# Kernel optimization log

Measured on AMD Instinct MI355X. Metric: run time of the kernel, lower is better.

## Reference

```python
import jax, jax.numpy as jnp
import numpy as np

DIM = 512
HEADS = 8
HD = DIM // HEADS          # head_dim = 64
GROUPS = 32                # GroupNorm groups
EPS = 1e-5
SCALE = HD ** -0.25        # double-scale: applied to both q and k
B, H, W, L, CTX = 8, 32, 32, 77, 768


def setup_inputs() -> dict:
    key = jax.random.key(0)
    ks = jax.random.split(key, 6)
    return {
        "x": jax.random.normal(ks[0], (B, DIM, H, W), jnp.float32),
        "context": jax.random.normal(ks[1], (B, L, CTX), jnp.float32),
        "gn_gamma": jnp.ones((DIM,), jnp.float32),
        "gn_beta": jnp.zeros((DIM,), jnp.float32),
        "qkv_w": jax.random.normal(ks[2], (3 * DIM, DIM), jnp.float32) * 0.02,
        "qkv_b": jnp.zeros((3 * DIM,), jnp.float32),
        "ckv_w": jax.random.normal(ks[3], (2 * DIM, CTX), jnp.float32) * 0.02,
        "ckv_b": jnp.zeros((2 * DIM,), jnp.float32),
        "proj_w": jax.random.normal(ks[4], (DIM, DIM), jnp.float32) * 0.02,
        "proj_b": jnp.zeros((DIM,), jnp.float32),
    }


def _group_norm(x, gamma, beta):
    b, c, h, w = x.shape
    xr = x.reshape(b, GROUPS, c // GROUPS, h, w)
    mu = xr.mean(axis=(2, 3, 4), keepdims=True)
    var = xr.var(axis=(2, 3, 4), keepdims=True)
    xr = (xr - mu) * jax.lax.rsqrt(var + EPS)
    return xr.reshape(b, c, h, w) * gamma[None, :, None, None] + beta[None, :, None, None]


def reference(x, context, gn_gamma, gn_beta, qkv_w, qkv_b, ckv_w, ckv_b, proj_w, proj_b):
    b, c, h, w = x.shape
    n, d = HEADS, HD
    identity = x

    xn = _group_norm(x, gn_gamma, gn_beta)
    # 1x1 conv == channel GEMM. qkv: [b, 3*dim, h*w] -> [b, 3, n, d, hw]
    qkv = jnp.einsum('bchw,oc->bohw', xn, qkv_w) + qkv_b[None, :, None, None]
    qkv = qkv.reshape(b, 3, n, d, h * w)
    q, k, v = qkv[:, 0], qkv[:, 1], qkv[:, 2]   # each [b, n, d, hw]

    # context kv: Linear(context_dim, 2*dim) -> [b, L, 2, n, d] -> [b, n, d, L]
    ckv = jnp.einsum('blc,oc->blo', context, ckv_w) + ckv_b
    ckv = ckv.reshape(b, -1, 2, n, d)
    ck = jnp.transpose(ckv[:, :, 0], (0, 2, 3, 1))  # [b, n, d, L]
    cv = jnp.transpose(ckv[:, :, 1], (0, 2, 3, 1))
    k = jnp.concatenate([ck, k], axis=-1)           # [b, n, d, L+hw]
    v = jnp.concatenate([cv, v], axis=-1)

    # attn = (q^T * s) @ (k * s); softmax over keys
    attn = jnp.einsum('bndq,bndk->bnqk', q * SCALE, k * SCALE)
    attn = jax.nn.softmax(attn, axis=-1)
    out = jnp.einsum('bndk,bnqk->bndq', v, attn).reshape(b, c, h, w)

    out = jnp.einsum('bchw,oc->bohw', out, proj_w) + proj_b[None, :, None, None]
    return out + identity
```

## Files before the change

### kernel.cpp

```cpp
#include <hip/hip_runtime.h>

#define B_ 8
#define DIM_ 512
#define HEADS_ 8
#define HD_ 64
#define HW_ 1024
#define L_ 77
#define LP_ 80
#define CTX_ 768
#define KV_ 1101
#define KVP_ 1152
#define NPAD_ 51
#define CTX0_ 1024
#define SC_QK 0.42466089f

typedef __attribute__((ext_vector_type(8))) short bf16x8;
typedef __attribute__((ext_vector_type(4))) float f32x4;
typedef __attribute__((ext_vector_type(4))) unsigned short u16x4;

__device__ __forceinline__ unsigned short f2bf(float f) {
  union { float f; unsigned int u; } c; c.f = f;
  unsigned int u = c.u;
  return (unsigned short)((u + 0x7fffu + ((u >> 16) & 1u)) >> 16);
}
__device__ __forceinline__ float bf2f(unsigned short h) {
  union { unsigned int u; float f; } c; c.u = ((unsigned int)h) << 16;
  return c.f;
}

#define GLD_LDS16(gsrc, ldst) \
  __builtin_amdgcn_global_load_lds((const __attribute__((address_space(1))) void*)(gsrc), \
                                   (__attribute__((address_space(3))) void*)(ldst), 16, 0, 0)

__global__ __launch_bounds__(256) void prep_k(const float* __restrict__ qkv_w,
                                              const float* __restrict__ ckv_w,
                                              const float* __restrict__ proj_w,
                                              const float* __restrict__ ctx,
                                              unsigned short* __restrict__ dq,
                                              unsigned short* __restrict__ dc,
                                              unsigned short* __restrict__ dp,
                                              unsigned short* __restrict__ ctx_bf,
                                              unsigned short* __restrict__ k_s,
                                              unsigned short* __restrict__ vT) {
  int bid = blockIdx.x;
  int tid = threadIdx.x;
  if (bid < 1792) {
    int i = bid * 256 + tid;
    const float* src;
    unsigned short* dst;
    int off;
    if (i < 196608) { src = qkv_w; dst = dq; off = i; }
    else if (i < 393216) { src = ckv_w; dst = dc; off = i - 196608; }
    else { src = proj_w; dst = dp; off = i - 393216; }
    float4 v = *(const float4*)(src + (size_t)off * 4);
    u16x4 o;
    o[0] = f2bf(v.x); o[1] = f2bf(v.y); o[2] = f2bf(v.z); o[3] = f2bf(v.w);
    *(u16x4*)(dst + (size_t)off * 4) = o;
  } else if (bid < 2272) {
    int i = (bid - 1792) * 256 + tid;
    int idx = i * 4;
    int b = idx / (LP_ * CTX_);
    int rem = idx - b * (LP_ * CTX_);
    int l = rem / CTX_;
    int c = rem - l * CTX_;
    float4 v = make_float4(0.f, 0.f, 0.f, 0.f);
    if (l < L_) v = *(const float4*)&ctx[((size_t)b * L_ + l) * CTX_ + c];
    u16x4 o;
    o[0] = f2bf(v.x); o[1] = f2bf(v.y); o[2] = f2bf(v.z); o[3] = f2bf(v.w);
    *(u16x4*)(ctx_bf + idx) = o;
  } else {
    int i = (bid - 2272) * 256 + tid;
    int bh = i / (NPAD_ * 64);
    int rem = i - bh * (NPAD_ * 64);
    int row = KV_ + rem / 64;
    int d = rem & 63;
    k_s[((size_t)bh * KVP_ + row) * HD_ + d] = 0;
    vT[((size_t)bh * HD_ + d) * KVP_ + row] = 0;
  }
}

__global__ __launch_bounds__(256) void gnorm_k(const float* __restrict__ x,
                                               const float* __restrict__ gamma,
                                               const float* __restrict__ beta,
                                               unsigned short* __restrict__ xn_t) {
  __shared__ unsigned short xs[16][1032];
  __shared__ float red[8];
  const int tid = threadIdx.x;
  const int b = blockIdx.x >> 5, g = blockIdx.x & 31;
  const float* xp = x + ((size_t)b * DIM_ + g * 16) * HW_;
  float sum = 0.f, ssq = 0.f;
#pragma unroll
  for (int i = 0; i < 16; ++i) {
    float4 v = *(const float4*)&xp[i * HW_ + tid * 4];
    sum += v.x + v.y + v.z + v.w;
    ssq += v.x * v.x + v.y * v.y + v.z * v.z + v.w * v.w;
    xs[i][tid * 4 + 0] = f2bf(v.x);
    xs[i][tid * 4 + 1] = f2bf(v.y);
    xs[i][tid * 4 + 2] = f2bf(v.z);
    xs[i][tid * 4 + 3] = f2bf(v.w);
  }
#pragma unroll
  for (int off = 32; off >= 1; off >>= 1) {
    sum += __shfl_xor(sum, off, 64);
    ssq += __shfl_xor(ssq, off, 64);
  }
  if ((tid & 63) == 0) { red[(tid >> 6) * 2] = sum; red[(tid >> 6) * 2 + 1] = ssq; }
  __syncthreads();
  sum = red[0] + red[2] + red[4] + red[6];
  ssq = red[1] + red[3] + red[5] + red[7];
  float mu = sum * (1.f / 16384.f);
  float rstd = rsqrtf(ssq * (1.f / 16384.f) - mu * mu + 1e-5f);
  float a[16], c[16];
#pragma unroll
  for (int ci = 0; ci < 16; ++ci) {
    float gm = gamma[g * 16 + ci], bt = beta[g * 16 + ci];
    a[ci] = rstd * gm;
    c[ci] = bt - mu * rstd * gm;
  }
#pragma unroll
  for (int t = 0; t < 4; ++t) {
    int hw = tid + t * 256;
    unsigned short tmp[16];
#pragma unroll
    for (int ci = 0; ci < 16; ++ci)
      tmp[ci] = f2bf(bf2f(xs[ci][hw]) * a[ci] + c[ci]);
    unsigned int w[8];
#pragma unroll
    for (int j = 0; j < 8; ++j) w[j] = (unsigned int)tmp[2 * j] | ((unsigned int)tmp[2 * j + 1] << 16);
    unsigned short* dptr = &xn_t[((size_t)b * HW_ + hw) * DIM_ + g * 16];
    *(uint4*)dptr = make_uint4(w[0], w[1], w[2], w[3]);
    *(uint4*)(dptr + 8) = make_uint4(w[4], w[5], w[6], w[7]);
  }
}

template <int MODE, int BM, int BN>
__device__ __forceinline__ void gemm_body(int bid,
                                          const unsigned short* __restrict__ A,
                                          const unsigned short* __restrict__ Bt,
                                          int M, int N, int K,
                                          const float* __restrict__ bias,
                                          unsigned short* __restrict__ out_q,
                                          unsigned short* __restrict__ out_k,
                                          unsigned short* __restrict__ out_v,
                                          const float* __restrict__ xres,
                                          float* __restrict__ outf,
                                          unsigned short* sm) {
  constexpr int MR = BM / 32;
  constexpr int NR = BN / 32;
  constexpr int SLOADS = BM / 32 + BN / 32;
  unsigned short* As0 = sm;
  unsigned short* Bs0 = sm + 2 * BM * 64;
  const int tid = threadIdx.x;
  const int wid = tid >> 6, lane = tid & 63;
  const int lr = lane & 15, lg = lane >> 4;
  const int ntn = N / BN;
  const int tm = bid / ntn, tn = bid - tm * ntn;
  const int m0 = tm * BM, n0 = tn * BN;
  const int wr = wid >> 1, wc = wid & 1;
  f32x4 acc[MR][NR] = {};
  const int nkt = K >> 6;

  auto stage = [&](int bi, int kk) {
#pragma unroll
    for (int i = 0; i < BM / 32; ++i) {
      int c = i * 256 + tid;
      int row = c >> 3, ch = (c & 7) ^ (row & 7);
      GLD_LDS16(A + (size_t)(m0 + row) * K + kk + ch * 8,
                As0 + (size_t)bi * BM * 64 + (size_t)(i * 256 + wid * 64) * 8);
    }
#pragma unroll
    for (int i = 0; i < BN / 32; ++i) {
      int c = i * 256 + tid;
      int row = c >> 3, ch = (c & 7) ^ (row & 7);
      GLD_LDS16(Bt + (size_t)(n0 + row) * K + kk + ch * 8,
                Bs0 + (size_t)bi * BN * 64 + (size_t)(i * 256 + wid * 64) * 8);
    }
  };

  __builtin_amdgcn_sched_barrier(0);
  stage(0, 0);
  __builtin_amdgcn_sched_barrier(0);
  if (nkt > 1) stage(1, 64);
  __builtin_amdgcn_sched_barrier(0);

  for (int kt = 0; kt < nkt; ++kt) {
    if (kt < nkt - 1) {
      if constexpr (SLOADS == 8)      asm volatile("s_waitcnt vmcnt(8)" ::: "memory");
      else if constexpr (SLOADS == 6) asm volatile("s_waitcnt vmcnt(6)" ::: "memory");
      else                            asm volatile("s_waitcnt vmcnt(0)" ::: "memory");
    } else {
      asm volatile("s_waitcnt vmcnt(0)" ::: "memory");
    }
    __builtin_amdgcn_sched_barrier(0);
    __builtin_amdgcn_s_barrier();
    __builtin_amdgcn_sched_barrier(0);
    const unsigned short* Ab = As0 + (kt & 1) * BM * 64;
    const unsigned short* Bb = Bs0 + (kt & 1) * BN * 64;
#pragma unroll
    for (int ks = 0; ks < 2; ++ks) {
      bf16x8 af[MR], bf[NR];
#pragma unroll
      for (int mi = 0; mi < MR; ++mi)
        af[mi] = *(const bf16x8*)&Ab[(wr * (BM / 2) + mi * 16 + lr) * 64 +
                                     (((ks * 4 + lg) ^ (lr & 7)) * 8)];
#pragma unroll
      for (int nj = 0; nj < NR; ++nj)
        bf[nj] = *(const bf16x8*)&Bb[(wc * (BN / 2) + nj * 16 + lr) * 64 +
                                     (((ks * 4 + lg) ^ (lr & 7)) * 8)];
#pragma unroll
      for (int mi = 0; mi < MR; ++mi)
#pragma unroll
        for (int nj = 0; nj < NR; ++nj)
          acc[mi][nj] = __builtin_amdgcn_mfma_f32_16x16x32_bf16(af[mi], bf[nj], acc[mi][nj], 0, 0, 0);
    }
    asm volatile("s_waitcnt lgkmcnt(0)" ::: "memory");
    __builtin_amdgcn_sched_barrier(0);
    __builtin_amdgcn_s_barrier();
    __builtin_amdgcn_sched_barrier(0);
    if (kt + 2 < nkt) stage(kt & 1, (kt + 2) << 6);
  }

  if constexpr (MODE == 0) {
    const int which = n0 >> 9;
    const int bb = m0 >> 10;
    const int qibase = m0 & 1023;
    if (which == 2) {
      uint2* Vt = (uint2*)sm;
#pragma unroll
      for (int mi = 0; mi < MR; ++mi) {
#pragma unroll
        for (int nj = 0; nj < NR; ++nj) {
          int col = wc * 64 + nj * 16 + lr;
          float b = bias[n0 + col];
          unsigned int w0, w1;
          float v0 = acc[mi][nj][0] + b, v1 = acc[mi][nj][1] + b;
          float v2 = acc[mi][nj][2] + b, v3 = acc[mi][nj][3] + b;
          asm("v_cvt_pk_bf16_f32 %0, %1, %2" : "=v"(w0) : "v"(v0), "v"(v1));
          asm("v_cvt_pk_bf16_f32 %0, %1, %2" : "=v"(w1) : "v"(v2), "v"(v3));
          int chunk = (wr * 16 + mi * 4 + lg) ^ (lr * 2);
          Vt[col * 32 + chunk] = make_uint2(w0, w1);
        }
      }
      __syncthreads();
#pragma unroll
      for (int it = 0; it < 8; ++it) {
        int col = wid * 32 + it * 4 + lg;
        uint4 val = *(uint4*)&Vt[col * 32 + ((lr * 2) ^ ((col & 15) * 2))];
        int colg = n0 + col;
        int head = (colg >> 6) & 7, d = colg & 63;
        *(uint4*)&out_v[(((size_t)bb * HEADS_ + head) * HD_ + d) * KVP_ + qibase + lr * 8] = val;
      }
    } else {
      unsigned short* Tq = sm;
#pragma unroll
      for (int mi = 0; mi < MR; ++mi) {
#pragma unroll
        for (int nj = 0; nj < NR; ++nj) {
          int col = wc * 64 + nj * 16 + lr;
          float b = bias[n0 + col];
          int qr = wr * 64 + mi * 16 + lg * 4;
#pragma unroll
          for (int r = 0; r < 4; ++r)
            Tq[(qr + r) * 132 + col] = f2bf((acc[mi][nj][r] + b) * SC_QK);
        }
      }
      __syncthreads();
#pragma unroll
      for (int it = 0; it < 8; ++it) {
        int qi = wid * 32 + it * 4 + lg;
        uint2 lo = *(uint2*)&Tq[qi * 132 + lr * 8];
        uint2 hi = *(uint2*)&Tq[qi * 132 + lr * 8 + 4];
        uint4 val = make_uint4(lo.x, lo.y, hi.x, hi.y);
        int colg = n0 + lr * 8;
        int head = (colg >> 6) & 7, d = colg & 63;
        size_t bh = (size_t)bb * HEADS_ + head;
        if (which == 0)
          *(uint4*)&out_q[(bh * HW_ + qibase + qi) * HD_ + d] = val;
        else
          *(uint4*)&out_k[(bh * KVP_ + qibase + qi) * HD_ + d] = val;
      }
    }
  } else {
#pragma unroll
    for (int mi = 0; mi < MR; ++mi) {
#pragma unroll
      for (int nj = 0; nj < NR; ++nj) {
#pragma unroll
        for (int r = 0; r < 4; ++r) {
          int row = m0 + wr * (BM / 2) + mi * 16 + lg * 4 + r;
          int col = n0 + wc * (BN / 2) + nj * 16 + lr;
          float v = acc[mi][nj][r];
          if (MODE == 1) {
            int bb = row / LP_, l = row - bb * LP_;
            if (l < L_) {
              v += bias[col];
              int which = col >> 9, head = (col >> 6) & 7, d = col & 63;
              size_t bh = (size_t)bb * HEADS_ + head;
              if (which == 0) out_k[(bh * KVP_ + CTX0_ + l) * HD_ + d] = f2bf(v * SC_QK);
              else            out_v[(bh * HD_ + d) * KVP_ + CTX0_ + l] = f2bf(v);
            }
          } else {
            size_t idx = (size_t)(col >> 10) * (DIM_ * HW_) + (size_t)row * HW_ + (col & 1023);
            outf[idx] = v + bias[row] + xres[idx];
          }
        }
      }
    }
  }
}

__global__ __launch_bounds__(256, 2) void gemm_qkv_ckv_k(
    const unsigned short* __restrict__ xn_t, const unsigned short* __restrict__ qkvw,
    const unsigned short* __restrict__ ctx_bf, const unsigned short* __restrict__ ckvw,
    const float* __restrict__ qkv_b, const float* __restrict__ ckv_b,
    unsigned short* __restrict__ q_s, unsigned short* __restrict__ k_s,
    unsigned short* __restrict__ vT) {
  __shared__ unsigned short sm[2 * 256 * 64];
  int bid = blockIdx.x;
  if (bid < 80) {
    gemm_body<1, 64, 128>(bid, ctx_bf, ckvw, 640, 1024, 768, ckv_b,
                          nullptr, k_s, vT, nullptr, nullptr, sm);
  } else {
    int b = bid - 80;
    int b2 = (b & 7) * 96 + (b >> 3);
    gemm_body<0, 128, 128>(b2, xn_t, qkvw, 8192, 1536, 512, qkv_b,
                           q_s, k_s, vT, nullptr, nullptr, sm);
  }
}

__global__ __launch_bounds__(256, 2) void gemm_proj_k(
    const unsigned short* __restrict__ projw, const unsigned short* __restrict__ at_s,
    const float* __restrict__ proj_b, const float* __restrict__ x,
    float* __restrict__ out) {
  __shared__ unsigned short sm[2 * 192 * 64];
  gemm_body<2, 64, 128>(blockIdx.x, projw, at_s, 512, 8192, 512, proj_b,
                        nullptr, nullptr, nullptr, x, out, sm);
}

#define PSTRIDE 72

__device__ __forceinline__ void attn_tile64(const unsigned short* __restrict__ Ksb,
                                            const unsigned short* __restrict__ Vsb,
                                            const bf16x8 (&qf)[2], const bf16x8 ones,
                                            unsigned short* __restrict__ Pw,
                                            int lr, int lg,
                                            const int (&ro)[4], const int (&koff)[2],
                                            f32x4& lacc, f32x4 (&acc)[4]) {
  f32x4 st[4] = {};
  __builtin_amdgcn_s_setprio(1);
#pragma unroll
  for (int ks = 0; ks < 2; ++ks) {
    bf16x8 kf[4];
#pragma unroll
    for (int t = 0; t < 4; ++t)
      kf[t] = *(const bf16x8*)&Ksb[ro[t] + koff[ks]];
#pragma unroll
    for (int t = 0; t < 4; ++t)
      st[t] = __builtin_amdgcn_mfma_f32_16x16x32_bf16(kf[t], qf[ks], st[t], 0, 0, 0);
  }
  __builtin_amdgcn_s_setprio(0);
#pragma unroll
  for (int t = 0; t < 4; ++t)
#pragma unroll
    for (int r = 0; r < 4; ++r) st[t][r] = __builtin_amdgcn_exp2f(st[t][r]);
#pragma unroll
  for (int t = 0; t < 4; ++t) {
    unsigned int w0, w1;
    asm("v_cvt_pk_bf16_f32 %0, %1, %2" : "=v"(w0) : "v"(st[t][0]), "v"(st[t][1]));
    asm("v_cvt_pk_bf16_f32 %0, %1, %2" : "=v"(w1) : "v"(st[t][2]), "v"(st[t][3]));
    *(uint2*)&Pw[lr * PSTRIDE + t * 16 + lg * 4] = make_uint2(w0, w1);
  }
#pragma unroll
  for (int ks = 0; ks < 2; ++ks) {
    bf16x8 pb = *(const bf16x8*)&Pw[lr * PSTRIDE + ks * 32 + lg * 8];
    __builtin_amdgcn_s_setprio(1);
    lacc = __builtin_amdgcn_mfma_f32_16x16x32_bf16(ones, pb, lacc, 0, 0, 0);
#pragma unroll
    for (int dt = 0; dt < 4; ++dt) {
      bf16x8 vf = *(const bf16x8*)&Vsb[ro[dt] + koff[ks]];
      acc[dt] = __builtin_amdgcn_mfma_f32_16x16x32_bf16(vf, pb, acc[dt], 0, 0, 0);
    }
    __builtin_amdgcn_s_setprio(0);
  }
}

__global__ __launch_bounds__(512, 4) void attn_k(const unsigned short* __restrict__ q_s,
                                                 const unsigned short* __restrict__ k_s,
                                                 const unsigned short* __restrict__ vT,
                                                 unsigned short* __restrict__ at_s) {
  __shared__ unsigned short Ks[2][4096];
  __shared__ unsigned short Vs[2][4096];
  __shared__ unsigned short Pb[8][16 * PSTRIDE];
  const int tid = threadIdx.x;
  const int wid = tid >> 6, lane = tid & 63;
  const int lr = lane & 15, lg = lane >> 4;
  const int bidx = blockIdx.x;
  const int xcd = bidx & 7, idx = bidx >> 3;
  const int bh = xcd + 8 * (idx >> 3);
  const int qt = idx & 7;
  const int q0 = qt * 128 + wid * 16;
  const unsigned short* qp = q_s + (size_t)bh * HW_ * HD_;
  const unsigned short* kp = k_s + (size_t)bh * KVP_ * HD_;
  const unsigned short* vp = vT + (size_t)bh * HD_ * KVP_;
  unsigned short* Pw = Pb[wid];

  const int srow = lane >> 3;
  const int schunk = (lane & 7) ^ srow;

  auto stage = [&](int bufi, int kk) {
    if (wid < 4) {
#pragma unroll
      for (int jj = 0; jj < 2; ++jj)
        GLD_LDS16(kp + (size_t)(kk + wid * 16 + jj * 8 + srow) * HD_ + schunk * 8,
                  &Ks[bufi][(wid * 2 + jj) * 512]);
    } else {
#pragma unroll
      for (int jj = 0; jj < 2; ++jj)
        GLD_LDS16(vp + (size_t)((wid - 4) * 16 + jj * 8 + srow) * KVP_ + kk + schunk * 8,
                  &Vs[bufi][((wid - 4) * 2 + jj) * 512]);
    }
  };

  int ro[4], koff[2];
#pragma unroll
  for (int t = 0; t < 4; ++t) ro[t] = (t * 16 + lr) * 64;
#pragma unroll
  for (int ks = 0; ks < 2; ++ks) koff[ks] = ((ks * 4 + lg) ^ (lr & 7)) * 8;

  bf16x8 qf[2];
#pragma unroll
  for (int ks = 0; ks < 2; ++ks)
    qf[ks] = *(const bf16x8*)&qp[(size_t)(q0 + lr) * HD_ + ks * 32 + lg * 8];

  bf16x8 ones;
#pragma unroll
  for (int j = 0; j < 8; ++j) ones[j] = (short)0x3F80;

  f32x4 acc[4] = {};
  f32x4 lacc = {};

  __builtin_amdgcn_sched_barrier(0);
  stage(0, 0);
  __builtin_amdgcn_sched_barrier(0);
  stage(1, 64);
  __builtin_amdgcn_sched_barrier(0);

  int cur = 0;
  for (int it = 0; it < 17; ++it) {
    asm volatile("s_waitcnt vmcnt(2)" ::: "memory");
    __builtin_amdgcn_sched_barrier(0);
    __builtin_amdgcn_s_barrier();
    __builtin_amdgcn_sched_barrier(0);
    attn_tile64(Ks[cur], Vs[cur], qf, ones, Pw, lr, lg, ro, koff, lacc, acc);
    asm volatile("s_waitcnt lgkmcnt(0)" ::: "memory");
    __builtin_amdgcn_sched_barrier(0);
    __builtin_amdgcn_s_barrier();
    __builtin_amdgcn_sched_barrier(0);
    if (it < 16) stage(cur, (it + 2) * 64);
    cur ^= 1;
  }
  asm volatile("s_waitcnt vmcnt(0)" ::: "memory");
  __builtin_amdgcn_sched_barrier(0);
  __builtin_amdgcn_s_barrier();
  __builtin_amdgcn_sched_barrier(0);
  attn_tile64(Ks[cur], Vs[cur], qf, ones, Pw, lr, lg, ro, koff, lacc, acc);

  const int bb = bh >> 3, head = bh & 7;
  const float inv = 1.f / (lacc[0] - (float)NPAD_);
  const int qi = q0 + lr;
#pragma unroll
  for (int dt = 0; dt < 4; ++dt) {
    u16x4 o;
#pragma unroll
    for (int r = 0; r < 4; ++r) o[r] = f2bf(acc[dt][r] * inv);
    *(u16x4*)&at_s[((size_t)bb * HW_ + qi) * DIM_ + head * HD_ + dt * 16 + lg * 4] = o;
  }
}

extern "C" void kernel_launch(void* const* d_in, const int* in_sizes, int n_in,
                              void* d_out, int out_size, void* d_ws, size_t ws_size,
                              hipStream_t stream) {
  (void)in_sizes; (void)n_in; (void)out_size; (void)ws_size;
  const float* x      = (const float*)d_in[0];
  const float* ctx    = (const float*)d_in[1];
  const float* gng    = (const float*)d_in[2];
  const float* gnb    = (const float*)d_in[3];
  const float* qkv_w  = (const float*)d_in[4];
  const float* qkv_b  = (const float*)d_in[5];
  const float* ckv_w  = (const float*)d_in[6];
  const float* ckv_b  = (const float*)d_in[7];
  const float* proj_w = (const float*)d_in[8];
  const float* proj_b = (const float*)d_in[9];
  float* out = (float*)d_out;

  char* ws = (char*)d_ws;
  size_t off = 0;
  auto alloc = [&](size_t bytes) {
    char* p = ws + off;
    off = (off + bytes + 255) & ~(size_t)255;
    return p;
  };
  unsigned short* xn_t    = (unsigned short*)alloc((size_t)B_ * HW_ * DIM_ * 2);
  unsigned short* ctx_bf  = (unsigned short*)alloc((size_t)B_ * LP_ * CTX_ * 2);
  unsigned short* qkvw_bf = (unsigned short*)alloc((size_t)3 * DIM_ * DIM_ * 2);
  unsigned short* ckvw_bf = (unsigned short*)alloc((size_t)2 * DIM_ * CTX_ * 2);
  unsigned short* projw_bf= (unsigned short*)alloc((size_t)DIM_ * DIM_ * 2);
  unsigned short* q_s     = (unsigned short*)alloc((size_t)64 * HW_ * HD_ * 2);
  unsigned short* k_s     = (unsigned short*)alloc((size_t)64 * KVP_ * HD_ * 2);
  unsigned short* vT      = (unsigned short*)alloc((size_t)64 * HD_ * KVP_ * 2);
  unsigned short* at_s    = (unsigned short*)alloc((size_t)B_ * HW_ * DIM_ * 2);

  prep_k<<<3088, 256, 0, stream>>>(qkv_w, ckv_w, proj_w, ctx,
                                   qkvw_bf, ckvw_bf, projw_bf, ctx_bf, k_s, vT);
  gnorm_k<<<256, 256, 0, stream>>>(x, gng, gnb, xn_t);
  gemm_qkv_ckv_k<<<848, 256, 0, stream>>>(xn_t, qkvw_bf, ctx_bf, ckvw_bf,
                                          qkv_b, ckv_b, q_s, k_s, vT);
  attn_k<<<512, 512, 0, stream>>>(q_s, k_s, vT, at_s);
  gemm_proj_k<<<512, 256, 0, stream>>>(projw_bf, at_s, proj_b, x, out);
}
```

Before: 75.67 us.

## Process two query tiles per wave in attention to reuse K/V fragments

```diff
diff --git a/kernel.cpp b/kernel.cpp
--- a/kernel.cpp
+++ b/kernel.cpp
@@ -341,12 +341,13 @@
 
 __device__ __forceinline__ void attn_tile64(const unsigned short* __restrict__ Ksb,
                                             const unsigned short* __restrict__ Vsb,
-                                            const bf16x8 (&qf)[2], const bf16x8 ones,
-                                            unsigned short* __restrict__ Pw,
+                                            const bf16x8 (&qf)[2][2], const bf16x8 ones,
+                                            unsigned short* __restrict__ Pw0,
+                                            unsigned short* __restrict__ Pw1,
                                             int lr, int lg,
                                             const int (&ro)[4], const int (&koff)[2],
-                                            f32x4& lacc, f32x4 (&acc)[4]) {
-  f32x4 st[4] = {};
+                                            f32x4 (&lacc)[2], f32x4 (&acc)[2][4]) {
+  f32x4 st[2][4] = {};
   __builtin_amdgcn_s_setprio(1);
 #pragma unroll
   for (int ks = 0; ks < 2; ++ks) {
@@ -355,42 +356,51 @@
     for (int t = 0; t < 4; ++t)
       kf[t] = *(const bf16x8*)&Ksb[ro[t] + koff[ks]];
 #pragma unroll
+    for (int t = 0; t < 4; ++t) {
+      st[0][t] = __builtin_amdgcn_mfma_f32_16x16x32_bf16(kf[t], qf[0][ks], st[0][t], 0, 0, 0);
+      st[1][t] = __builtin_amdgcn_mfma_f32_16x16x32_bf16(kf[t], qf[1][ks], st[1][t], 0, 0, 0);
+    }
+  }
+  __builtin_amdgcn_s_setprio(0);
+#pragma unroll
+  for (int c = 0; c < 2; ++c) {
+#pragma unroll
     for (int t = 0; t < 4; ++t)
-      st[t] = __builtin_amdgcn_mfma_f32_16x16x32_bf16(kf[t], qf[ks], st[t], 0, 0, 0);
-  }
-  __builtin_amdgcn_s_setprio(0);
-#pragma unroll
-  for (int t = 0; t < 4; ++t)
-#pragma unroll
-    for (int r = 0; r < 4; ++r) st[t][r] = __builtin_amdgcn_exp2f(st[t][r]);
-#pragma unroll
-  for (int t = 0; t < 4; ++t) {
-    unsigned int w0, w1;
-    asm("v_cvt_pk_bf16_f32 %0, %1, %2" : "=v"(w0) : "v"(st[t][0]), "v"(st[t][1]));
-    asm("v_cvt_pk_bf16_f32 %0, %1, %2" : "=v"(w1) : "v"(st[t][2]), "v"(st[t][3]));
-    *(uint2*)&Pw[lr * PSTRIDE + t * 16 + lg * 4] = make_uint2(w0, w1);
+#pragma unroll
+      for (int r = 0; r < 4; ++r) st[c][t][r] = __builtin_amdgcn_exp2f(st[c][t][r]);
+    unsigned short* Pw = c ? Pw1 : Pw0;
+#pragma unroll
+    for (int t = 0; t < 4; ++t) {
+      unsigned int w0, w1;
+      asm("v_cvt_pk_bf16_f32 %0, %1, %2" : "=v"(w0) : "v"(st[c][t][0]), "v"(st[c][t][1]));
+      asm("v_cvt_pk_bf16_f32 %0, %1, %2" : "=v"(w1) : "v"(st[c][t][2]), "v"(st[c][t][3]));
+      *(uint2*)&Pw[lr * PSTRIDE + t * 16 + lg * 4] = make_uint2(w0, w1);
+    }
   }
 #pragma unroll
   for (int ks = 0; ks < 2; ++ks) {
-    bf16x8 pb = *(const bf16x8*)&Pw[lr * PSTRIDE + ks * 32 + lg * 8];
+    bf16x8 pb0 = *(const bf16x8*)&Pw0[lr * PSTRIDE + ks * 32 + lg * 8];
+    bf16x8 pb1 = *(const bf16x8*)&Pw1[lr * PSTRIDE + ks * 32 + lg * 8];
     __builtin_amdgcn_s_setprio(1);
-    lacc = __builtin_amdgcn_mfma_f32_16x16x32_bf16(ones, pb, lacc, 0, 0, 0);
+    lacc[0] = __builtin_amdgcn_mfma_f32_16x16x32_bf16(ones, pb0, lacc[0], 0, 0, 0);
+    lacc[1] = __builtin_amdgcn_mfma_f32_16x16x32_bf16(ones, pb1, lacc[1], 0, 0, 0);
 #pragma unroll
     for (int dt = 0; dt < 4; ++dt) {
       bf16x8 vf = *(const bf16x8*)&Vsb[ro[dt] + koff[ks]];
-      acc[dt] = __builtin_amdgcn_mfma_f32_16x16x32_bf16(vf, pb, acc[dt], 0, 0, 0);
+      acc[0][dt] = __builtin_amdgcn_mfma_f32_16x16x32_bf16(vf, pb0, acc[0][dt], 0, 0, 0);
+      acc[1][dt] = __builtin_amdgcn_mfma_f32_16x16x32_bf16(vf, pb1, acc[1][dt], 0, 0, 0);
     }
     __builtin_amdgcn_s_setprio(0);
   }
 }
 
-__global__ __launch_bounds__(512, 4) void attn_k(const unsigned short* __restrict__ q_s,
+__global__ __launch_bounds__(256, 3) void attn_k(const unsigned short* __restrict__ q_s,
                                                  const unsigned short* __restrict__ k_s,
                                                  const unsigned short* __restrict__ vT,
                                                  unsigned short* __restrict__ at_s) {
   __shared__ unsigned short Ks[2][4096];
   __shared__ unsigned short Vs[2][4096];
-  __shared__ unsigned short Pb[8][16 * PSTRIDE];
+  __shared__ unsigned short Pb[4][2][16 * PSTRIDE];
   const int tid = threadIdx.x;
   const int wid = tid >> 6, lane = tid & 63;
   const int lr = lane & 15, lg = lane >> 4;
@@ -398,26 +408,23 @@
   const int xcd = bidx & 7, idx = bidx >> 3;
   const int bh = xcd + 8 * (idx >> 3);
   const int qt = idx & 7;
-  const int q0 = qt * 128 + wid * 16;
+  const int q0 = qt * 128 + wid * 32;
   const unsigned short* qp = q_s + (size_t)bh * HW_ * HD_;
   const unsigned short* kp = k_s + (size_t)bh * KVP_ * HD_;
   const unsigned short* vp = vT + (size_t)bh * HD_ * KVP_;
-  unsigned short* Pw = Pb[wid];
+  unsigned short* Pw0 = Pb[wid][0];
+  unsigned short* Pw1 = Pb[wid][1];
 
   const int srow = lane >> 3;
   const int schunk = (lane & 7) ^ srow;
 
   auto stage = [&](int bufi, int kk) {
-    if (wid < 4) {
-#pragma unroll
-      for (int jj = 0; jj < 2; ++jj)
-        GLD_LDS16(kp + (size_t)(kk + wid * 16 + jj * 8 + srow) * HD_ + schunk * 8,
-                  &Ks[bufi][(wid * 2 + jj) * 512]);
-    } else {
-#pragma unroll
-      for (int jj = 0; jj < 2; ++jj)
-        GLD_LDS16(vp + (size_t)((wid - 4) * 16 + jj * 8 + srow) * KVP_ + kk + schunk * 8,
-                  &Vs[bufi][((wid - 4) * 2 + jj) * 512]);
+#pragma unroll
+    for (int jj = 0; jj < 2; ++jj) {
+      GLD_LDS16(kp + (size_t)(kk + wid * 16 + jj * 8 + srow) * HD_ + schunk * 8,
+                &Ks[bufi][(wid * 2 + jj) * 512]);
+      GLD_LDS16(vp + (size_t)(wid * 16 + jj * 8 + srow) * KVP_ + kk + schunk * 8,
+                &Vs[bufi][(wid * 2 + jj) * 512]);
     }
   };
 
@@ -427,17 +434,19 @@
 #pragma unroll
   for (int ks = 0; ks < 2; ++ks) koff[ks] = ((ks * 4 + lg) ^ (lr & 7)) * 8;
 
-  bf16x8 qf[2];
-#pragma unroll
-  for (int ks = 0; ks < 2; ++ks)
-    qf[ks] = *(const bf16x8*)&qp[(size_t)(q0 + lr) * HD_ + ks * 32 + lg * 8];
+  bf16x8 qf[2][2];
+#pragma unroll
+  for (int c = 0; c < 2; ++c)
+#pragma unroll
+    for (int ks = 0; ks < 2; ++ks)
+      qf[c][ks] = *(const bf16x8*)&qp[(size_t)(q0 + c * 16 + lr) * HD_ + ks * 32 + lg * 8];
 
   bf16x8 ones;
 #pragma unroll
   for (int j = 0; j < 8; ++j) ones[j] = (short)0x3F80;
 
-  f32x4 acc[4] = {};
-  f32x4 lacc = {};
+  f32x4 acc[2][4] = {};
+  f32x4 lacc[2] = {};
 
   __builtin_amdgcn_sched_barrier(0);
   stage(0, 0);
@@ -447,11 +456,11 @@
 
   int cur = 0;
   for (int it = 0; it < 17; ++it) {
-    asm volatile("s_waitcnt vmcnt(2)" ::: "memory");
+    asm volatile("s_waitcnt vmcnt(4)" ::: "memory");
     __builtin_amdgcn_sched_barrier(0);
     __builtin_amdgcn_s_barrier();
     __builtin_amdgcn_sched_barrier(0);
-    attn_tile64(Ks[cur], Vs[cur], qf, ones, Pw, lr, lg, ro, koff, lacc, acc);
+    attn_tile64(Ks[cur], Vs[cur], qf, ones, Pw0, Pw1, lr, lg, ro, koff, lacc, acc);
     asm volatile("s_waitcnt lgkmcnt(0)" ::: "memory");
     __builtin_amdgcn_sched_barrier(0);
     __builtin_amdgcn_s_barrier();
@@ -463,17 +472,20 @@
   __builtin_amdgcn_sched_barrier(0);
   __builtin_amdgcn_s_barrier();
   __builtin_amdgcn_sched_barrier(0);
-  attn_tile64(Ks[cur], Vs[cur], qf, ones, Pw, lr, lg, ro, koff, lacc, acc);
+  attn_tile64(Ks[cur], Vs[cur], qf, ones, Pw0, Pw1, lr, lg, ro, koff, lacc, acc);
 
   const int bb = bh >> 3, head = bh & 7;
-  const float inv = 1.f / (lacc[0] - (float)NPAD_);
-  const int qi = q0 + lr;
-#pragma unroll
-  for (int dt = 0; dt < 4; ++dt) {
-    u16x4 o;
-#pragma unroll
-    for (int r = 0; r < 4; ++r) o[r] = f2bf(acc[dt][r] * inv);
-    *(u16x4*)&at_s[((size_t)bb * HW_ + qi) * DIM_ + head * HD_ + dt * 16 + lg * 4] = o;
+#pragma unroll
+  for (int c = 0; c < 2; ++c) {
+    const float inv = 1.f / (lacc[c][0] - (float)NPAD_);
+    const int qi = q0 + c * 16 + lr;
+#pragma unroll
+    for (int dt = 0; dt < 4; ++dt) {
+      u16x4 o;
+#pragma unroll
+      for (int r = 0; r < 4; ++r) o[r] = f2bf(acc[c][dt][r] * inv);
+      *(u16x4*)&at_s[((size_t)bb * HW_ + qi) * DIM_ + head * HD_ + dt * 16 + lg * 4] = o;
+    }
   }
 }
 
@@ -515,6 +527,6 @@
   gnorm_k<<<256, 256, 0, stream>>>(x, gng, gnb, xn_t);
   gemm_qkv_ckv_k<<<848, 256, 0, stream>>>(xn_t, qkvw_bf, ctx_bf, ckvw_bf,
                                           qkv_b, ckv_b, q_s, k_s, vT);
-  attn_k<<<512, 512, 0, stream>>>(q_s, k_s, vT, at_s);
+  attn_k<<<512, 256, 0, stream>>>(q_s, k_s, vT, at_s);
   gemm_proj_k<<<512, 256, 0, stream>>>(projw_bf, at_s, proj_b, x, out);
 }
```

After: 74.82 us. No clear change (-1.1%).
